# Performance work log

Measured on AMD Instinct MI355X. Metric: run time of the kernel, lower is better.

Reference implementation:

```python
import jax, jax.numpy as jnp
import numpy as np

NX, NQ, NU, NY = 256, 64, 8, 4
N = 65536
EPS = 0.01
STD = 0.5


def setup_inputs() -> dict:
    key = jax.random.key(0)
    ks = jax.random.split(key, 8)
    return {
        "x": jax.random.normal(ks[0], (N, NX), jnp.float32),
        "u": jax.random.normal(ks[1], (N, NU), jnp.float32),
        "X": jax.random.normal(ks[2], (NX + NQ, NX + NQ), jnp.float32) * STD,
        "U": jax.random.normal(ks[3], (NX, NQ), jnp.float32) * STD,
        "Y1": jax.random.normal(ks[4], (NX, NX), jnp.float32) * STD,
        "XP": jax.random.normal(ks[5], (NX, NX), jnp.float32) * STD,
        "B2": jax.random.normal(ks[6], (NX, NU), jnp.float32) * STD,
        "D12": jax.random.normal(ks[7], (NQ, NU), jnp.float32) * STD,
        "bv": jnp.zeros((NQ,), jnp.float32),
        "t": 0,
    }


def _constrained(X, U, Y1, XP):
    # updateParameters(): build A, B1, C1, D11 from unconstrained params.
    P = XP @ XP.T + EPS * jnp.eye(NX, dtype=XP.dtype)
    H = X @ X.T + EPS * jnp.eye(NX + NQ, dtype=X.dtype)
    H11, H12, H22 = H[:NX, :NX], H[:NX, NX:], H[NX:, NX:]
    Y = -0.5 * (H11 + Y1 - Y1.T)
    Pinv = jnp.linalg.inv(P)
    A = Pinv @ Y                                   # [nx, nx]
    lam = 0.5 * jnp.diagonal(H22)                  # Lambda diagonal
    D11 = -jnp.tril(H22, -1) / lam[:, None]        # strictly lower triangular [nq, nq]
    C1 = U.T / lam[:, None]                        # [nq, nx]
    B1 = Pinv @ (-H12 - U)                         # [nx, nq]
    return A, B1, C1, D11


def _calc_w(base, D11):
    # Forward substitution: w_i = relu(base_i + sum_{j<i} D11[i,j] * w_j).
    # D11 is strictly lower triangular and unfilled w columns are zero, so a
    # full matvec against the carry is exact.
    nq = base.shape[1]

    def step(w, inp):
        i, row, b_col = inp                        # row: [nq], b_col: [Nbatch]
        wi = jax.nn.relu(b_col + w @ row)
        return w.at[:, i].set(wi), None

    w0 = jnp.zeros_like(base)
    w, _ = jax.lax.scan(step, w0, (jnp.arange(nq), D11, base.T))
    return w


def reference(x, u, X, U, Y1, XP, B2, D12, bv, t):
    A, B1, C1, D11 = _constrained(X, U, Y1, XP)
    base = x @ C1.T + u @ D12.T + bv               # [N, nq]
    w = _calc_w(base, D11)
    x_dot = x @ A.T + w @ B1.T + u @ B2.T          # [N, nx]
    return x_dot
```

## Files before the change

### kernel.cpp

```cpp
#include <hip/hip_runtime.h>

#define EPS_C 0.01f

typedef __attribute__((ext_vector_type(8))) short short8;
typedef __attribute__((ext_vector_type(4))) float f32x4;
typedef __attribute__((ext_vector_type(4))) unsigned short u16x4;
typedef __attribute__((ext_vector_type(8))) unsigned short u16x8;

#define WS_H    0
#define WS_C    102400
#define WS_C2   167936
#define WS_Y    233472
#define WS_RHS  299008
#define WS_D11  331776
#define WS_WFH  419840
#define WS_WFM  464896
#define WS_WFL  509952
#define WS_BBH  555008
#define WS_BBM  564224
#define WS_BBL  573440
#define WS_WG   582656
#define WS_E    4776960

__device__ __forceinline__ unsigned short f2bf(float f) {
    unsigned int u = __float_as_uint(f);
    unsigned int r = (u + 0x7fffu + ((u >> 16) & 1u)) >> 16;
    return (unsigned short)r;
}
__device__ __forceinline__ float bf2f(unsigned short h) {
    return __uint_as_float(((unsigned int)h) << 16);
}
__device__ __forceinline__ void split1(float f, unsigned short& h, unsigned short& m, unsigned short& l) {
    h = f2bf(f);
    float r1 = f - bf2f(h);
    m = f2bf(r1);
    l = f2bf(r1 - bf2f(m));
}
__device__ __forceinline__ void split8(const float* v, short8& h8, short8& m8, short8& l8) {
#pragma unroll
    for (int j = 0; j < 8; ++j) {
        unsigned short h, m, l;
        split1(v[j], h, m, l);
        h8[j] = (short)h; m8[j] = (short)m; l8[j] = (short)l;
    }
}

__global__ void k_build(const float* __restrict__ Xm, const float* __restrict__ XPm,
                        float* __restrict__ H, float* __restrict__ P) {
    int idx = blockIdx.x * 256 + threadIdx.x;
    if (idx < 102400) {
        int i = idx / 320, j = idx - i * 320;
        const float4* a = (const float4*)(Xm + i * 320);
        const float4* b = (const float4*)(Xm + j * 320);
        float s = 0.f;
        for (int k = 0; k < 80; ++k) {
            float4 va = a[k], vb = b[k];
            s += va.x * vb.x + va.y * vb.y + va.z * vb.z + va.w * vb.w;
        }
        H[idx] = (i == j) ? s + EPS_C : s;
    } else {
        idx -= 102400;
        if (idx < 65536) {
            int i = idx >> 8, j = idx & 255;
            const float4* a = (const float4*)(XPm + i * 256);
            const float4* b = (const float4*)(XPm + j * 256);
            float s = 0.f;
            for (int k = 0; k < 64; ++k) {
                float4 va = a[k], vb = b[k];
                s += va.x * vb.x + va.y * vb.y + va.z * vb.z + va.w * vb.w;
            }
            P[idx] = (i == j) ? s + EPS_C : s;
        }
    }
}

__global__ void k_derived(const float* __restrict__ H, const float* __restrict__ Um,
                          const float* __restrict__ Y1, const float* __restrict__ B2,
                          const float* __restrict__ D12,
                          float* __restrict__ Y, float* __restrict__ RHS,
                          float* __restrict__ D11g,
                          unsigned short* __restrict__ Bh, unsigned short* __restrict__ Bm,
                          unsigned short* __restrict__ Bl,
                          unsigned short* __restrict__ Bbh, unsigned short* __restrict__ Bbm,
                          unsigned short* __restrict__ Bbl) {
    int idx = blockIdx.x * 256 + threadIdx.x;
    if (idx < 65536) {
        int i = idx >> 8, j = idx & 255;
        Y[idx] = -0.5f * (H[i * 320 + j] + Y1[i * 256 + j] - Y1[j * 256 + i]);
        return;
    }
    idx -= 65536;
    if (idx < 16384) {
        RHS[idx] = -H[(idx >> 6) * 320 + 256 + (idx & 63)] - Um[idx];
        return;
    }
    idx -= 16384;
    if (idx < 4096) {
        int q = idx >> 6, j = idx & 63;
        float lam = 0.5f * H[(256 + q) * 320 + 256 + q];
        D11g[idx] = (j < q) ? -H[(256 + q) * 320 + 256 + j] / lam : 0.f;
        return;
    }
    idx -= 4096;
    if (idx < 8192) {
        int o = idx >> 5, cc = idx & 31;
        float f = (cc < 8) ? B2[o * 8 + cc] : 0.f;
        unsigned short h, m, l;
        split1(f, h, m, l);
        size_t off = (size_t)o * 352 + 256 + cc;
        Bh[off] = h; Bm[off] = m; Bl[off] = l;
        return;
    }
    idx -= 8192;
    if (idx < 18432) {
        int q = idx / 288, k = idx - q * 288;
        float f;
        if (k < 256) {
            float lam = 0.5f * H[(256 + q) * 320 + 256 + q];
            f = Um[(size_t)k * 64 + q] / lam;
        } else if (k < 264) f = D12[(size_t)q * 8 + (k - 256)];
        else f = 0.f;
        unsigned short h, m, l;
        split1(f, h, m, l);
        Bbh[idx] = h; Bbm[idx] = m; Bbl[idx] = l;
    }
}

__global__ void __launch_bounds__(256) k_inv8(const float* __restrict__ Cold, float* __restrict__ E, int b) {
    __shared__ __align__(16) float M[64 * 68];
    __shared__ __align__(16) float Rs[8 * 68];
    __shared__ __align__(16) float Ts[64 * 8];
    __shared__ float E8s[8 * 9];
    const int tid = threadIdx.x;
    const int ti = tid & 15, tj = tid >> 4;
#pragma unroll
    for (int t = 0; t < 4; ++t) {
        int e = tid + t * 256;
        int r = e >> 4, c4 = e & 15;
        float4 v = *(const float4*)&Cold[(size_t)(b * 64 + r) * 256 + b * 64 + c4 * 4];
        *(float4*)&M[r * 68 + c4 * 4] = v;
    }
    __syncthreads();
    for (int s = 0; s < 8; ++s) {
        if (tid < 64) {
            const int lane = tid;
            float e8[8];
#pragma unroll
            for (int j = 0; j < 8; ++j) e8[j] = 0.f;
            if (lane < 8) {
#pragma unroll
                for (int j = 0; j < 8; ++j) e8[j] = M[(s * 8 + lane) * 68 + s * 8 + j];
            }
#pragma unroll
            for (int k = 0; k < 8; ++k) {
                const float p = __shfl(e8[k], k);
                const float rinv = 1.0f / p;
                const float f = -e8[k] * rinv;
                const bool isk = (lane == k);
#pragma unroll
                for (int j = 0; j < 8; ++j) {
                    const float prj = __shfl(e8[j], k);
                    if (j == k) e8[j] = isk ? rinv : f;
                    else        e8[j] = isk ? prj * rinv : fmaf(f, prj, e8[j]);
                }
            }
            if (lane < 8) {
#pragma unroll
                for (int j = 0; j < 8; ++j) E8s[lane * 9 + j] = e8[j];
            }
        }
        __syncthreads();
#pragma unroll
        for (int t = 0; t < 2; ++t) {
            int e = tid + t * 256;
            int r = e >> 6, c = e & 63;
            Rs[r * 68 + c] = M[(s * 8 + r) * 68 + c];
        }
#pragma unroll
        for (int t = 0; t < 2; ++t) {
            int e = tid + t * 256;
            int i = e >> 3, c = e & 7;
            float acc = 0.f;
#pragma unroll
            for (int j = 0; j < 8; ++j) acc = fmaf(M[i * 68 + s * 8 + j], E8s[j * 9 + c], acc);
            Ts[i * 8 + c] = acc;
        }
        __syncthreads();
        {
            const bool rowIn = ((ti >> 1) == s);
            const bool colIn = ((tj >> 1) == s);
            const int i0 = ti * 4, j0 = tj * 4;
            float nv[4][4];
            if (rowIn && colIn) {
#pragma unroll
                for (int r = 0; r < 4; ++r)
#pragma unroll
                    for (int d = 0; d < 4; ++d)
                        nv[r][d] = E8s[(i0 - s * 8 + r) * 9 + (j0 - s * 8 + d)];
            } else if (rowIn) {
#pragma unroll
                for (int r = 0; r < 4; ++r)
#pragma unroll
                    for (int d = 0; d < 4; ++d) {
                        float acc = 0.f;
#pragma unroll
                        for (int c = 0; c < 8; ++c)
                            acc = fmaf(E8s[(i0 - s * 8 + r) * 9 + c], Rs[c * 68 + j0 + d], acc);
                        nv[r][d] = acc;
                    }
            } else if (colIn) {
#pragma unroll
                for (int r = 0; r < 4; ++r)
#pragma unroll
                    for (int d = 0; d < 4; ++d)
                        nv[r][d] = -Ts[(i0 + r) * 8 + (j0 - s * 8 + d)];
            } else {
#pragma unroll
                for (int r = 0; r < 4; ++r)
#pragma unroll
                    for (int d = 0; d < 4; ++d) {
                        float acc = M[(i0 + r) * 68 + j0 + d];
#pragma unroll
                        for (int c = 0; c < 8; ++c)
                            acc = fmaf(-Ts[(i0 + r) * 8 + c], Rs[c * 68 + j0 + d], acc);
                        nv[r][d] = acc;
                    }
            }
#pragma unroll
            for (int r = 0; r < 4; ++r)
#pragma unroll
                for (int d = 0; d < 4; ++d) M[(i0 + r) * 68 + j0 + d] = nv[r][d];
        }
        __syncthreads();
    }
#pragma unroll
    for (int t = 0; t < 4; ++t) {
        int e = tid + t * 256;
        int r = e >> 4, c4 = e & 15;
        float4 v = *(const float4*)&M[r * 68 + c4 * 4];
        *(float4*)&E[(size_t)r * 64 + c4 * 4] = v;
    }
}

__global__ void __launch_bounds__(256) k_gjS(const float* __restrict__ Cold, float* __restrict__ Cnew,
                                             float* __restrict__ E, int b, int nb) {
    const int I = blockIdx.x >> 2, J = blockIdx.x & 3;
    const int tid = threadIdx.x;
    const int ti = tid & 15, tj = tid >> 4;
    if (I == b && J == b) {
        const int r = tid >> 2, seg = tid & 3;
#pragma unroll
        for (int t = 0; t < 4; ++t) {
            float4 v = *(const float4*)&E[(size_t)r * 64 + seg * 16 + t * 4];
            *(float4*)&Cnew[(size_t)(b * 64 + r) * 256 + b * 64 + seg * 16 + t * 4] = v;
        }
        return;
    }
    __shared__ __align__(16) float Es[64 * 68];
    __shared__ __align__(16) float S1[64 * 68];
    __shared__ __align__(16) float S2[64 * 68];
    for (int e = tid; e < 1024; e += 256) {
        int r = e >> 4, c4 = e & 15;
        float4 v = *(const float4*)&E[(size_t)r * 64 + c4 * 4];
        *(float4*)&Es[r * 68 + c4 * 4] = v;
    }
    if (I == b) {
        for (int e = tid; e < 1024; e += 256) {
            int r = e >> 4, c4 = e & 15;
            float4 v = *(const float4*)&Cold[(size_t)(b * 64 + r) * 256 + J * 64 + c4 * 4];
            *(float4*)&S1[r * 68 + c4 * 4] = v;
        }
        __syncthreads();
        float acc[4][4];
#pragma unroll
        for (int r = 0; r < 4; ++r)
#pragma unroll
            for (int d = 0; d < 4; ++d) acc[r][d] = 0.f;
        for (int mm = 0; mm < 64; ++mm) {
            float a4[4], b4[4];
#pragma unroll
            for (int d = 0; d < 4; ++d) { a4[d] = Es[(ti * 4 + d) * 68 + mm]; b4[d] = S1[mm * 68 + tj * 4 + d]; }
#pragma unroll
            for (int r = 0; r < 4; ++r)
#pragma unroll
                for (int d = 0; d < 4; ++d) acc[r][d] = fmaf(a4[r], b4[d], acc[r][d]);
        }
#pragma unroll
        for (int r = 0; r < 4; ++r) {
            float4 v = {acc[r][0], acc[r][1], acc[r][2], acc[r][3]};
            *(float4*)&Cnew[(size_t)(b * 64 + ti * 4 + r) * 256 + J * 64 + tj * 4] = v;
        }
        return;
    }
    if (J == b) {
        for (int e = tid; e < 1024; e += 256) {
            int r = e >> 4, c4 = e & 15;
            float4 v = *(const float4*)&Cold[(size_t)(I * 64 + r) * 256 + b * 64 + c4 * 4];
            *(float4*)&S1[r * 68 + c4 * 4] = v;
        }
        __syncthreads();
        float acc[4][4];
#pragma unroll
        for (int r = 0; r < 4; ++r)
#pragma unroll
            for (int d = 0; d < 4; ++d) acc[r][d] = 0.f;
        for (int kk = 0; kk < 64; ++kk) {
            float a4[4], b4[4];
#pragma unroll
            for (int d = 0; d < 4; ++d) { a4[d] = S1[(ti * 4 + d) * 68 + kk]; b4[d] = Es[kk * 68 + tj * 4 + d]; }
#pragma unroll
            for (int r = 0; r < 4; ++r)
#pragma unroll
                for (int d = 0; d < 4; ++d) acc[r][d] = fmaf(a4[r], b4[d], acc[r][d]);
        }
#pragma unroll
        for (int r = 0; r < 4; ++r) {
            float4 v = {-acc[r][0], -acc[r][1], -acc[r][2], -acc[r][3]};
            *(float4*)&Cnew[(size_t)(I * 64 + ti * 4 + r) * 256 + b * 64 + tj * 4] = v;
        }
        return;
    }
    for (int e = tid; e < 1024; e += 256) {
        int r = e >> 4, c4 = e & 15;
        float4 v = *(const float4*)&Cold[(size_t)(I * 64 + r) * 256 + b * 64 + c4 * 4];
        *(float4*)&S1[r * 68 + c4 * 4] = v;
        float4 w = *(const float4*)&Cold[(size_t)(b * 64 + r) * 256 + J * 64 + c4 * 4];
        *(float4*)&S2[r * 68 + c4 * 4] = w;
    }
    __syncthreads();
    float t4[4][4];
#pragma unroll
    for (int r = 0; r < 4; ++r)
#pragma unroll
        for (int d = 0; d < 4; ++d) t4[r][d] = 0.f;
    for (int kk = 0; kk < 64; ++kk) {
        float a4[4], b4[4];
#pragma unroll
        for (int d = 0; d < 4; ++d) { a4[d] = S1[(ti * 4 + d) * 68 + kk]; b4[d] = Es[kk * 68 + tj * 4 + d]; }
#pragma unroll
        for (int r = 0; r < 4; ++r)
#pragma unroll
            for (int d = 0; d < 4; ++d) t4[r][d] = fmaf(a4[r], b4[d], t4[r][d]);
    }
    __syncthreads();
#pragma unroll
    for (int r = 0; r < 4; ++r)
#pragma unroll
        for (int d = 0; d < 4; ++d) S1[(ti * 4 + r) * 68 + tj * 4 + d] = t4[r][d];
    __syncthreads();
    float acc[4][4];
#pragma unroll
    for (int r = 0; r < 4; ++r) {
        float4 cv = *(const float4*)&Cold[(size_t)(I * 64 + ti * 4 + r) * 256 + J * 64 + tj * 4];
        acc[r][0] = cv.x; acc[r][1] = cv.y; acc[r][2] = cv.z; acc[r][3] = cv.w;
    }
    for (int kk = 0; kk < 64; ++kk) {
        float a4[4], b4[4];
#pragma unroll
        for (int d = 0; d < 4; ++d) { a4[d] = S1[(ti * 4 + d) * 68 + kk]; b4[d] = S2[kk * 68 + tj * 4 + d]; }
#pragma unroll
        for (int r = 0; r < 4; ++r)
#pragma unroll
            for (int d = 0; d < 4; ++d) acc[r][d] = fmaf(-a4[r], b4[d], acc[r][d]);
    }
#pragma unroll
    for (int r = 0; r < 4; ++r) {
        float4 v = {acc[r][0], acc[r][1], acc[r][2], acc[r][3]};
        *(float4*)&Cnew[(size_t)(I * 64 + ti * 4 + r) * 256 + J * 64 + tj * 4] = v;
    }
    if (I == nb && J == nb) {
        float* M   = Es;
        float* Rs2 = S2;
        float* Ts2 = S2 + 1024;
        float* E8s = S2 + 1664;
        __syncthreads();
#pragma unroll
        for (int r = 0; r < 4; ++r)
#pragma unroll
            for (int d = 0; d < 4; ++d)
                M[(ti * 4 + r) * 68 + tj * 4 + d] = acc[r][d];
        __syncthreads();
        for (int s = 0; s < 8; ++s) {
            if (tid < 64) {
                const int lane = tid;
                float e8[8];
#pragma unroll
                for (int j = 0; j < 8; ++j) e8[j] = 0.f;
                if (lane < 8) {
#pragma unroll
                    for (int j = 0; j < 8; ++j) e8[j] = M[(s * 8 + lane) * 68 + s * 8 + j];
                }
#pragma unroll
                for (int k = 0; k < 8; ++k) {
                    const float p = __shfl(e8[k], k);
                    const float rinv = 1.0f / p;
                    const float f = -e8[k] * rinv;
                    const bool isk = (lane == k);
#pragma unroll
                    for (int j = 0; j < 8; ++j) {
                        const float prj = __shfl(e8[j], k);
                        if (j == k) e8[j] = isk ? rinv : f;
                        else        e8[j] = isk ? prj * rinv : fmaf(f, prj, e8[j]);
                    }
                }
                if (lane < 8) {
#pragma unroll
                    for (int j = 0; j < 8; ++j) E8s[lane * 9 + j] = e8[j];
                }
            }
            __syncthreads();
#pragma unroll
            for (int t = 0; t < 2; ++t) {
                int e = tid + t * 256;
                int r = e >> 6, c = e & 63;
                Rs2[r * 68 + c] = M[(s * 8 + r) * 68 + c];
            }
#pragma unroll
            for (int t = 0; t < 2; ++t) {
                int e = tid + t * 256;
                int i = e >> 3, c = e & 7;
                float a2 = 0.f;
#pragma unroll
                for (int j = 0; j < 8; ++j) a2 = fmaf(M[i * 68 + s * 8 + j], E8s[j * 9 + c], a2);
                Ts2[i * 8 + c] = a2;
            }
            __syncthreads();
            {
                const bool rowIn = ((ti >> 1) == s);
                const bool colIn = ((tj >> 1) == s);
                const int i0 = ti * 4, j0 = tj * 4;
                float nv[4][4];
                if (rowIn && colIn) {
#pragma unroll
                    for (int r = 0; r < 4; ++r)
#pragma unroll
                        for (int d = 0; d < 4; ++d)
                            nv[r][d] = E8s[(i0 - s * 8 + r) * 9 + (j0 - s * 8 + d)];
                } else if (rowIn) {
#pragma unroll
                    for (int r = 0; r < 4; ++r)
#pragma unroll
                        for (int d = 0; d < 4; ++d) {
                            float a2 = 0.f;
#pragma unroll
                            for (int c = 0; c < 8; ++c)
                                a2 = fmaf(E8s[(i0 - s * 8 + r) * 9 + c], Rs2[c * 68 + j0 + d], a2);
                            nv[r][d] = a2;
                        }
                } else if (colIn) {
#pragma unroll
                    for (int r = 0; r < 4; ++r)
#pragma unroll
                        for (int d = 0; d < 4; ++d)
                            nv[r][d] = -Ts2[(i0 + r) * 8 + (j0 - s * 8 + d)];
                } else {
#pragma unroll
                    for (int r = 0; r < 4; ++r)
#pragma unroll
                        for (int d = 0; d < 4; ++d) {
                            float a2 = M[(i0 + r) * 68 + j0 + d];
#pragma unroll
                            for (int c = 0; c < 8; ++c)
                                a2 = fmaf(-Ts2[(i0 + r) * 8 + c], Rs2[c * 68 + j0 + d], a2);
                            nv[r][d] = a2;
                        }
                }
#pragma unroll
                for (int r = 0; r < 4; ++r)
#pragma unroll
                    for (int d = 0; d < 4; ++d) M[(i0 + r) * 68 + j0 + d] = nv[r][d];
            }
            __syncthreads();
        }
#pragma unroll
        for (int t = 0; t < 4; ++t) {
            int e = tid + t * 256;
            int r = e >> 4, c4 = e & 15;
            float4 v = *(const float4*)&M[r * 68 + c4 * 4];
            *(float4*)&E[(size_t)r * 64 + c4 * 4] = v;
        }
    }
}

__global__ void __launch_bounds__(256) k_apply2(const float* __restrict__ PI, const float* __restrict__ Y,
                                                const float* __restrict__ RHS,
                                                unsigned short* __restrict__ Bh, unsigned short* __restrict__ Bm,
                                                unsigned short* __restrict__ Bl) {
    const int i0 = ((int)blockIdx.x / 5) * 64;
    const int c0 = ((int)blockIdx.x % 5) * 64;
    __shared__ __align__(16) float S1[64 * 68], S2[64 * 68];
    const int tid = threadIdx.x;
    const int ti = tid & 15, tj = tid >> 4;
    float acc[4][4];
#pragma unroll
    for (int r = 0; r < 4; ++r)
#pragma unroll
        for (int d = 0; d < 4; ++d) acc[r][d] = 0.f;
    for (int kc = 0; kc < 4; ++kc) {
        __syncthreads();
        for (int e = tid; e < 1024; e += 256) {
            int i = e >> 4, k4 = e & 15;
            float4 v = *(const float4*)&PI[(size_t)(i0 + i) * 256 + kc * 64 + k4 * 4];
            S1[(k4 * 4 + 0) * 68 + i] = v.x;
            S1[(k4 * 4 + 1) * 68 + i] = v.y;
            S1[(k4 * 4 + 2) * 68 + i] = v.z;
            S1[(k4 * 4 + 3) * 68 + i] = v.w;
            float4 w;
            if (c0 < 256) w = *(const float4*)&Y[(size_t)(kc * 64 + i) * 256 + c0 + k4 * 4];
            else          w = *(const float4*)&RHS[(size_t)(kc * 64 + i) * 64 + k4 * 4];
            *(float4*)&S2[i * 68 + k4 * 4] = w;
        }
        __syncthreads();
        for (int kk = 0; kk < 64; ++kk) {
            float4 pv = *(const float4*)&S1[kk * 68 + ti * 4];
            float4 gv = *(const float4*)&S2[kk * 68 + tj * 4];
            float p4[4] = {pv.x, pv.y, pv.z, pv.w};
            float g4[4] = {gv.x, gv.y, gv.z, gv.w};
#pragma unroll
            for (int r = 0; r < 4; ++r)
#pragma unroll
                for (int d = 0; d < 4; ++d) acc[r][d] = fmaf(p4[r], g4[d], acc[r][d]);
        }
    }
    const int pc0 = (c0 < 256) ? c0 : 288;
#pragma unroll
    for (int r = 0; r < 4; ++r)
#pragma unroll
        for (int d = 0; d < 4; ++d) {
            unsigned short h, m, l;
            split1(acc[r][d], h, m, l);
            size_t off = (size_t)(i0 + ti * 4 + r) * 352 + pc0 + tj * 4 + d;
            Bh[off] = h; Bm[off] = m; Bl[off] = l;
        }
}

#define XSTR 264
__global__ void __launch_bounds__(256, 3) k_base(const float* __restrict__ x, const float* __restrict__ u,
                                                 const unsigned short* __restrict__ Bbh,
                                                 const unsigned short* __restrict__ Bbm,
                                                 const unsigned short* __restrict__ Bbl,
                                                 const float* __restrict__ bv,
                                                 float* __restrict__ wg) {
    __shared__ __align__(16) unsigned short Ah[32 * XSTR];
    __shared__ __align__(16) unsigned short Am[32 * XSTR];
    __shared__ __align__(16) unsigned short Al[32 * XSTR];
    const int tid = threadIdx.x;
    const int r0 = blockIdx.x * 32;
    {
        const float4* xg4 = (const float4*)(x + (size_t)r0 * 256);
#pragma unroll
        for (int i = 0; i < 8; ++i) {
            int e = tid + i * 256, r = e >> 6, c4 = e & 63;
            float4 v = xg4[e];
            float vv[4] = {v.x, v.y, v.z, v.w};
            u16x4 hv, mv, lv;
#pragma unroll
            for (int j = 0; j < 4; ++j) {
                unsigned short h, m, l;
                split1(vv[j], h, m, l);
                hv[j] = h; mv[j] = m; lv[j] = l;
            }
            *(u16x4*)&Ah[r * XSTR + c4 * 4] = hv;
            *(u16x4*)&Am[r * XSTR + c4 * 4] = mv;
            *(u16x4*)&Al[r * XSTR + c4 * 4] = lv;
        }
    }
    __syncthreads();
    const int lane = tid & 63, wid = tid >> 6;
    const int n0 = wid * 16;
    const int lr = lane & 15, lg = lane >> 4;
    const int lk = lg * 8;
    const int noff = (n0 + lr) * 288;
    f32x4 acc[2];
    acc[0] = (f32x4){0.f, 0.f, 0.f, 0.f};
    acc[1] = (f32x4){0.f, 0.f, 0.f, 0.f};
    short8 cb_h, nb_h, b_m, b_l;
    cb_h = *(const short8*)&Bbh[noff + lk];
#pragma unroll
    for (int kt = 0; kt < 9; ++kt) {
        const int ka = kt * 32 + lk;
        b_m = *(const short8*)&Bbm[noff + ka];
        b_l = *(const short8*)&Bbl[noff + ka];
        if (kt < 8) nb_h = *(const short8*)&Bbh[noff + ka + 32];
        short8 a_h[2], a_m[2], a_l[2];
        if (kt < 8) {
            a_h[0] = *(const short8*)&Ah[lr * XSTR + ka];
            a_h[1] = *(const short8*)&Ah[(16 + lr) * XSTR + ka];
            a_m[0] = *(const short8*)&Am[lr * XSTR + ka];
            a_m[1] = *(const short8*)&Am[(16 + lr) * XSTR + ka];
            a_l[0] = *(const short8*)&Al[lr * XSTR + ka];
            a_l[1] = *(const short8*)&Al[(16 + lr) * XSTR + ka];
        } else {
            if (lg == 0) {
                float vv[8];
                const float4* up = (const float4*)&u[(size_t)(r0 + lr) * 8];
                float4 v0 = up[0], v1 = up[1];
                vv[0] = v0.x; vv[1] = v0.y; vv[2] = v0.z; vv[3] = v0.w;
                vv[4] = v1.x; vv[5] = v1.y; vv[6] = v1.z; vv[7] = v1.w;
                split8(vv, a_h[0], a_m[0], a_l[0]);
                const float4* up2 = (const float4*)&u[(size_t)(r0 + 16 + lr) * 8];
                float4 w0 = up2[0], w1 = up2[1];
                vv[0] = w0.x; vv[1] = w0.y; vv[2] = w0.z; vv[3] = w0.w;
                vv[4] = w1.x; vv[5] = w1.y; vv[6] = w1.z; vv[7] = w1.w;
                split8(vv, a_h[1], a_m[1], a_l[1]);
            } else {
                short8 z = {0, 0, 0, 0, 0, 0, 0, 0};
                a_h[0] = z; a_h[1] = z; a_m[0] = z; a_m[1] = z; a_l[0] = z; a_l[1] = z;
            }
        }
#pragma unroll
        for (int m = 0; m < 2; ++m) {
            acc[m] = __builtin_amdgcn_mfma_f32_16x16x32_bf16(a_h[m], cb_h, acc[m], 0, 0, 0);
            acc[m] = __builtin_amdgcn_mfma_f32_16x16x32_bf16(a_m[m], cb_h, acc[m], 0, 0, 0);
            acc[m] = __builtin_amdgcn_mfma_f32_16x16x32_bf16(a_l[m], cb_h, acc[m], 0, 0, 0);
        }
#pragma unroll
        for (int m = 0; m < 2; ++m) {
            acc[m] = __builtin_amdgcn_mfma_f32_16x16x32_bf16(a_h[m], b_m, acc[m], 0, 0, 0);
            acc[m] = __builtin_amdgcn_mfma_f32_16x16x32_bf16(a_m[m], b_m, acc[m], 0, 0, 0);
        }
#pragma unroll
        for (int m = 0; m < 2; ++m)
            acc[m] = __builtin_amdgcn_mfma_f32_16x16x32_bf16(a_h[m], b_l, acc[m], 0, 0, 0);
        if (kt < 8) cb_h = nb_h;
    }
    const float bvv = bv[n0 + lr];
#pragma unroll
    for (int m = 0; m < 2; ++m)
#pragma unroll
        for (int j = 0; j < 4; ++j)
            wg[(size_t)(r0 + m * 16 + lg * 4 + j) * 64 + n0 + lr] = acc[m][j] + bvv;
}

__global__ void __launch_bounds__(256) k_rec(float* __restrict__ wg, const float* __restrict__ D11g) {
    __shared__ float D[64 * 64];
    const int tid = threadIdx.x;
#pragma unroll
    for (int t = 0; t < 16; ++t) D[tid + t * 256] = D11g[tid + t * 256];
    __syncthreads();
    const size_t r = (size_t)blockIdx.x * 256 + tid;
    float w[64];
    float* wr = wg + r * 64;
#pragma unroll
    for (int c = 0; c < 16; ++c) {
        float4 v = *(const float4*)&wr[c * 4];
        w[4 * c] = v.x; w[4 * c + 1] = v.y; w[4 * c + 2] = v.z; w[4 * c + 3] = v.w;
    }
    w[0] = fmaxf(w[0], 0.f);
#pragma unroll
    for (int i = 1; i < 64; ++i) {
        float s0 = w[i], s1 = 0.f, s2 = 0.f, s3 = 0.f;
#pragma unroll
        for (int j = 0; j + 3 < i; j += 4) {
            s0 = fmaf(w[j + 0], D[i * 64 + j + 0], s0);
            s1 = fmaf(w[j + 1], D[i * 64 + j + 1], s1);
            s2 = fmaf(w[j + 2], D[i * 64 + j + 2], s2);
            s3 = fmaf(w[j + 3], D[i * 64 + j + 3], s3);
        }
#pragma unroll
        for (int j = i & ~3; j < i; ++j) s0 = fmaf(w[j], D[i * 64 + j], s0);
        w[i] = fmaxf((s0 + s1) + (s2 + s3), 0.f);
    }
#pragma unroll
    for (int c = 0; c < 16; ++c) {
        float4 v = {w[4 * c], w[4 * c + 1], w[4 * c + 2], w[4 * c + 3]};
        *(float4*)&wr[c * 4] = v;
    }
}

__global__ void __launch_bounds__(256, 3) k_m2(const float* __restrict__ x, const float* __restrict__ wg,
                                               const float* __restrict__ u,
                                               const unsigned short* __restrict__ Bh,
                                               const unsigned short* __restrict__ Bm,
                                               const unsigned short* __restrict__ Bl,
                                               float* __restrict__ out) {
    __shared__ __align__(16) unsigned short Ah[32 * XSTR];
    __shared__ __align__(16) unsigned short Am[32 * XSTR];
    __shared__ __align__(16) unsigned short Al[32 * XSTR];
    const int tid = threadIdx.x;
    const int r0 = blockIdx.x * 32;
    {
        const float4* xg4 = (const float4*)(x + (size_t)r0 * 256);
#pragma unroll
        for (int i = 0; i < 8; ++i) {
            int e = tid + i * 256, r = e >> 6, c4 = e & 63;
            float4 v = xg4[e];
            float vv[4] = {v.x, v.y, v.z, v.w};
            u16x4 hv, mv, lv;
#pragma unroll
            for (int j = 0; j < 4; ++j) {
                unsigned short h, m, l;
                split1(vv[j], h, m, l);
                hv[j] = h; mv[j] = m; lv[j] = l;
            }
            *(u16x4*)&Ah[r * XSTR + c4 * 4] = hv;
            *(u16x4*)&Am[r * XSTR + c4 * 4] = mv;
            *(u16x4*)&Al[r * XSTR + c4 * 4] = lv;
        }
    }
    __syncthreads();
    const int lane = tid & 63, wid = tid >> 6;
    const int n0 = wid * 64;
    const int lr = lane & 15, lg = lane >> 4;
    const int lk = lg * 8;
    int noff[4];
#pragma unroll
    for (int nf = 0; nf < 4; ++nf) noff[nf] = (n0 + nf * 16 + lr) * 352;
    f32x4 acc[2][4];
#pragma unroll
    for (int m = 0; m < 2; ++m)
#pragma unroll
        for (int nf = 0; nf < 4; ++nf) acc[m][nf] = (f32x4){0.f, 0.f, 0.f, 0.f};
    short8 cb_h[4], nb_h[4], b_m[4], b_l[4];
#pragma unroll
    for (int nf = 0; nf < 4; ++nf) cb_h[nf] = *(const short8*)&Bh[noff[nf] + lk];
#pragma unroll
    for (int kt = 0; kt < 11; ++kt) {
        const int ka = kt * 32 + lk;
#pragma unroll
        for (int nf = 0; nf < 4; ++nf) b_m[nf] = *(const short8*)&Bm[noff[nf] + ka];
#pragma unroll
        for (int nf = 0; nf < 4; ++nf) b_l[nf] = *(const short8*)&Bl[noff[nf] + ka];
        if (kt < 10) {
#pragma unroll
            for (int nf = 0; nf < 4; ++nf) nb_h[nf] = *(const short8*)&Bh[noff[nf] + ka + 32];
        }
        short8 a_h[2], a_m[2], a_l[2];
        if (kt < 8) {
            a_h[0] = *(const short8*)&Ah[lr * XSTR + ka];
            a_h[1] = *(const short8*)&Ah[(16 + lr) * XSTR + ka];
            a_m[0] = *(const short8*)&Am[lr * XSTR + ka];
            a_m[1] = *(const short8*)&Am[(16 + lr) * XSTR + ka];
            a_l[0] = *(const short8*)&Al[lr * XSTR + ka];
            a_l[1] = *(const short8*)&Al[(16 + lr) * XSTR + ka];
        } else if (kt == 8) {
            if (lg == 0) {
                float vv[8];
                const float4* up = (const float4*)&u[(size_t)(r0 + lr) * 8];
                float4 v0 = up[0], v1 = up[1];
                vv[0] = v0.x; vv[1] = v0.y; vv[2] = v0.z; vv[3] = v0.w;
                vv[4] = v1.x; vv[5] = v1.y; vv[6] = v1.z; vv[7] = v1.w;
                split8(vv, a_h[0], a_m[0], a_l[0]);
                const float4* up2 = (const float4*)&u[(size_t)(r0 + 16 + lr) * 8];
                float4 w0 = up2[0], w1 = up2[1];
                vv[0] = w0.x; vv[1] = w0.y; vv[2] = w0.z; vv[3] = w0.w;
                vv[4] = w1.x; vv[5] = w1.y; vv[6] = w1.z; vv[7] = w1.w;
                split8(vv, a_h[1], a_m[1], a_l[1]);
            } else {
                short8 z = {0, 0, 0, 0, 0, 0, 0, 0};
                a_h[0] = z; a_h[1] = z; a_m[0] = z; a_m[1] = z; a_l[0] = z; a_l[1] = z;
            }
        } else {
            const int wc = (kt - 9) * 32 + lk;
            float vv[8];
            const float4* wp = (const float4*)&wg[(size_t)(r0 + lr) * 64 + wc];
            float4 v0 = wp[0], v1 = wp[1];
            vv[0] = v0.x; vv[1] = v0.y; vv[2] = v0.z; vv[3] = v0.w;
            vv[4] = v1.x; vv[5] = v1.y; vv[6] = v1.z; vv[7] = v1.w;
            split8(vv, a_h[0], a_m[0], a_l[0]);
            const float4* wp2 = (const float4*)&wg[(size_t)(r0 + 16 + lr) * 64 + wc];
            float4 w0 = wp2[0], w1 = wp2[1];
            vv[0] = w0.x; vv[1] = w0.y; vv[2] = w0.z; vv[3] = w0.w;
            vv[4] = w1.x; vv[5] = w1.y; vv[6] = w1.z; vv[7] = w1.w;
            split8(vv, a_h[1], a_m[1], a_l[1]);
        }
#pragma unroll
        for (int nf = 0; nf < 4; ++nf)
#pragma unroll
            for (int m = 0; m < 2; ++m) {
                acc[m][nf] = __builtin_amdgcn_mfma_f32_16x16x32_bf16(a_h[m], cb_h[nf], acc[m][nf], 0, 0, 0);
                acc[m][nf] = __builtin_amdgcn_mfma_f32_16x16x32_bf16(a_m[m], cb_h[nf], acc[m][nf], 0, 0, 0);
                acc[m][nf] = __builtin_amdgcn_mfma_f32_16x16x32_bf16(a_l[m], cb_h[nf], acc[m][nf], 0, 0, 0);
            }
#pragma unroll
        for (int nf = 0; nf < 4; ++nf)
#pragma unroll
            for (int m = 0; m < 2; ++m) {
                acc[m][nf] = __builtin_amdgcn_mfma_f32_16x16x32_bf16(a_h[m], b_m[nf], acc[m][nf], 0, 0, 0);
                acc[m][nf] = __builtin_amdgcn_mfma_f32_16x16x32_bf16(a_m[m], b_m[nf], acc[m][nf], 0, 0, 0);
                if (kt >= 9)
                    acc[m][nf] = __builtin_amdgcn_mfma_f32_16x16x32_bf16(a_l[m], b_m[nf], acc[m][nf], 0, 0, 0);
            }
#pragma unroll
        for (int nf = 0; nf < 4; ++nf)
#pragma unroll
            for (int m = 0; m < 2; ++m) {
                acc[m][nf] = __builtin_amdgcn_mfma_f32_16x16x32_bf16(a_h[m], b_l[nf], acc[m][nf], 0, 0, 0);
                if (kt >= 9)
                    acc[m][nf] = __builtin_amdgcn_mfma_f32_16x16x32_bf16(a_m[m], b_l[nf], acc[m][nf], 0, 0, 0);
            }
        if (kt < 10) {
#pragma unroll
            for (int nf = 0; nf < 4; ++nf) cb_h[nf] = nb_h[nf];
        }
    }
#pragma unroll
    for (int m = 0; m < 2; ++m)
#pragma unroll
        for (int nf = 0; nf < 4; ++nf)
#pragma unroll
            for (int j = 0; j < 4; ++j)
                out[(size_t)(r0 + m * 16 + lg * 4 + j) * 256 + n0 + nf * 16 + lr] = acc[m][nf][j];
}

extern "C" void kernel_launch(void* const* d_in, const int* in_sizes, int n_in,
                              void* d_out, int out_size, void* d_ws, size_t ws_size,
                              hipStream_t stream) {
    const float* x   = (const float*)d_in[0];
    const float* u   = (const float*)d_in[1];
    const float* Xm  = (const float*)d_in[2];
    const float* Um  = (const float*)d_in[3];
    const float* Y1  = (const float*)d_in[4];
    const float* XPm = (const float*)d_in[5];
    const float* B2  = (const float*)d_in[6];
    const float* D12 = (const float*)d_in[7];
    const float* bv  = (const float*)d_in[8];
    float* out = (float*)d_out;
    float* ws  = (float*)d_ws;

    float* H    = ws + WS_H;
    float* C0   = ws + WS_C;
    float* C1   = ws + WS_C2;
    float* Y    = ws + WS_Y;
    float* RHS  = ws + WS_RHS;
    float* D11g = ws + WS_D11;
    float* E    = ws + WS_E;
    unsigned short* Bh  = (unsigned short*)(ws + WS_WFH);
    unsigned short* Bm  = (unsigned short*)(ws + WS_WFM);
    unsigned short* Bl  = (unsigned short*)(ws + WS_WFL);
    unsigned short* Bbh = (unsigned short*)(ws + WS_BBH);
    unsigned short* Bbm = (unsigned short*)(ws + WS_BBM);
    unsigned short* Bbl = (unsigned short*)(ws + WS_BBL);
    float* wg = ws + WS_WG;

    k_build<<<656, 256, 0, stream>>>(Xm, XPm, H, C0);
    k_derived<<<441, 256, 0, stream>>>(H, Um, Y1, B2, D12, Y, RHS, D11g,
                                       Bh, Bm, Bl, Bbh, Bbm, Bbl);
    k_base<<<2048, 256, 0, stream>>>(x, u, Bbh, Bbm, Bbl, bv, wg);
    k_rec<<<256, 256, 0, stream>>>(wg, D11g);
    k_inv8<<<1, 256, 0, stream>>>(C0, E, 0);
    k_gjS<<<16, 256, 0, stream>>>(C0, C1, E, 0, 1);
    k_gjS<<<16, 256, 0, stream>>>(C1, C0, E, 1, 2);
    k_gjS<<<16, 256, 0, stream>>>(C0, C1, E, 2, 3);
    k_gjS<<<16, 256, 0, stream>>>(C1, C0, E, 3, -1);
    k_apply2<<<20, 256, 0, stream>>>(C0, Y, RHS, Bh, Bm, Bl);
    k_m2<<<2048, 256, 0, stream>>>(x, wg, u, Bh, Bm, Bl, out);
}
```

Before: 373.6 us.

## Pre-swizzle split-bf16 weight fragments into MFMA order and double-buffer GJ pivot block

Weight split arrays (Bh/Bm/Bl and Bbh/Bbm/Bbl) are now stored in a fragment-tiled layout matching the 16x16x32 MFMA operand order, so each lane's 8-element load is contiguous and coalesced instead of striding across 352/288-element rows. The k_m2 and k_base loops drop the manual prefetch of the next high part and load all three parts per k-tile. The MFMA term order is regrouped, and the last two k-tiles of k_m2 now include the a_m·b_l and a_l·b_m terms. The Gauss-Jordan pivot inverse E is ping-ponged between two buffers to avoid a read/write hazard across blocks. Dropping the software prefetch may expose global load latency.

After: 340.7 us. -8.8%, faster.

```diff
diff --git a/kernel.cpp b/kernel.cpp
--- a/kernel.cpp
+++ b/kernel.cpp
@@ -20,7 +20,15 @@
 #define WS_BBM  564224
 #define WS_BBL  573440
 #define WS_WG   582656
-#define WS_E    4776960
+#define WS_E0   4776960
+#define WS_E1   4781056
+
+__device__ __forceinline__ int wfoff(int n, int k) {
+    return (((n >> 4) * 44 + (k >> 5) * 4 + ((k >> 3) & 3)) << 7) + ((n & 15) << 3) + (k & 7);
+}
+__device__ __forceinline__ int bboff(int n, int k) {
+    return (((n >> 4) * 36 + (k >> 5) * 4 + ((k >> 3) & 3)) << 7) + ((n & 15) << 3) + (k & 7);
+}
 
 __device__ __forceinline__ unsigned short f2bf(float f) {
     unsigned int u = __float_as_uint(f);
@@ -107,7 +115,7 @@
         float f = (cc < 8) ? B2[o * 8 + cc] : 0.f;
         unsigned short h, m, l;
         split1(f, h, m, l);
-        size_t off = (size_t)o * 352 + 256 + cc;
+        int off = wfoff(o, 256 + cc);
         Bh[off] = h; Bm[off] = m; Bl[off] = l;
         return;
     }
@@ -122,7 +130,8 @@
         else f = 0.f;
         unsigned short h, m, l;
         split1(f, h, m, l);
-        Bbh[idx] = h; Bbm[idx] = m; Bbl[idx] = l;
+        int off = bboff(q, k);
+        Bbh[off] = h; Bbm[off] = m; Bbl[off] = l;
     }
 }
 
@@ -243,7 +252,8 @@
 }
 
 __global__ void __launch_bounds__(256) k_gjS(const float* __restrict__ Cold, float* __restrict__ Cnew,
-                                             float* __restrict__ E, int b, int nb) {
+                                             const float* __restrict__ E, float* __restrict__ Eout,
+                                             int b, int nb) {
     const int I = blockIdx.x >> 2, J = blockIdx.x & 3;
     const int tid = threadIdx.x;
     const int ti = tid & 15, tj = tid >> 4;
@@ -477,7 +487,7 @@
             int e = tid + t * 256;
             int r = e >> 4, c4 = e & 15;
             float4 v = *(const float4*)&M[r * 68 + c4 * 4];
-            *(float4*)&E[(size_t)r * 64 + c4 * 4] = v;
+            *(float4*)&Eout[(size_t)r * 64 + c4 * 4] = v;
         }
     }
 }
@@ -529,7 +539,7 @@
         for (int d = 0; d < 4; ++d) {
             unsigned short h, m, l;
             split1(acc[r][d], h, m, l);
-            size_t off = (size_t)(i0 + ti * 4 + r) * 352 + pc0 + tj * 4 + d;
+            int off = wfoff(i0 + ti * 4 + r, pc0 + tj * 4 + d);
             Bh[off] = h; Bm[off] = m; Bl[off] = l;
         }
 }
@@ -570,18 +580,12 @@
     const int n0 = wid * 16;
     const int lr = lane & 15, lg = lane >> 4;
     const int lk = lg * 8;
-    const int noff = (n0 + lr) * 288;
+    const int fb = wid * 4608 + lg * 128 + lr * 8;
     f32x4 acc[2];
     acc[0] = (f32x4){0.f, 0.f, 0.f, 0.f};
     acc[1] = (f32x4){0.f, 0.f, 0.f, 0.f};
-    short8 cb_h, nb_h, b_m, b_l;
-    cb_h = *(const short8*)&Bbh[noff + lk];
-#pragma unroll
     for (int kt = 0; kt < 9; ++kt) {
         const int ka = kt * 32 + lk;
-        b_m = *(const short8*)&Bbm[noff + ka];
-        b_l = *(const short8*)&Bbl[noff + ka];
-        if (kt < 8) nb_h = *(const short8*)&Bbh[noff + ka + 32];
         short8 a_h[2], a_m[2], a_l[2];
         if (kt < 8) {
             a_h[0] = *(const short8*)&Ah[lr * XSTR + ka];
@@ -608,21 +612,19 @@
                 a_h[0] = z; a_h[1] = z; a_m[0] = z; a_m[1] = z; a_l[0] = z; a_l[1] = z;
             }
         }
+        const int off = fb + kt * 512;
+        short8 b_h = *(const short8*)&Bbh[off];
+        short8 b_m = *(const short8*)&Bbm[off];
+        short8 b_l = *(const short8*)&Bbl[off];
 #pragma unroll
         for (int m = 0; m < 2; ++m) {
-            acc[m] = __builtin_amdgcn_mfma_f32_16x16x32_bf16(a_h[m], cb_h, acc[m], 0, 0, 0);
-            acc[m] = __builtin_amdgcn_mfma_f32_16x16x32_bf16(a_m[m], cb_h, acc[m], 0, 0, 0);
-            acc[m] = __builtin_amdgcn_mfma_f32_16x16x32_bf16(a_l[m], cb_h, acc[m], 0, 0, 0);
-        }
-#pragma unroll
-        for (int m = 0; m < 2; ++m) {
+            acc[m] = __builtin_amdgcn_mfma_f32_16x16x32_bf16(a_h[m], b_h, acc[m], 0, 0, 0);
+            acc[m] = __builtin_amdgcn_mfma_f32_16x16x32_bf16(a_m[m], b_h, acc[m], 0, 0, 0);
             acc[m] = __builtin_amdgcn_mfma_f32_16x16x32_bf16(a_h[m], b_m, acc[m], 0, 0, 0);
+            acc[m] = __builtin_amdgcn_mfma_f32_16x16x32_bf16(a_l[m], b_h, acc[m], 0, 0, 0);
             acc[m] = __builtin_amdgcn_mfma_f32_16x16x32_bf16(a_m[m], b_m, acc[m], 0, 0, 0);
-        }
-#pragma unroll
-        for (int m = 0; m < 2; ++m)
             acc[m] = __builtin_amdgcn_mfma_f32_16x16x32_bf16(a_h[m], b_l, acc[m], 0, 0, 0);
-        if (kt < 8) cb_h = nb_h;
+        }
     }
     const float bvv = bv[n0 + lr];
 #pragma unroll
@@ -703,55 +705,81 @@
     const int n0 = wid * 64;
     const int lr = lane & 15, lg = lane >> 4;
     const int lk = lg * 8;
-    int noff[4];
-#pragma unroll
-    for (int nf = 0; nf < 4; ++nf) noff[nf] = (n0 + nf * 16 + lr) * 352;
+    const int lgoff = lg * 128 + lr * 8;
+    int fb[4];
+#pragma unroll
+    for (int nf = 0; nf < 4; ++nf) fb[nf] = (wid * 4 + nf) * 5632 + lgoff;
     f32x4 acc[2][4];
 #pragma unroll
     for (int m = 0; m < 2; ++m)
 #pragma unroll
         for (int nf = 0; nf < 4; ++nf) acc[m][nf] = (f32x4){0.f, 0.f, 0.f, 0.f};
-    short8 cb_h[4], nb_h[4], b_m[4], b_l[4];
-#pragma unroll
-    for (int nf = 0; nf < 4; ++nf) cb_h[nf] = *(const short8*)&Bh[noff[nf] + lk];
-#pragma unroll
-    for (int kt = 0; kt < 11; ++kt) {
+
+#define M2_MFMA6()                                                                               \
+    for (int nf = 0; nf < 4; ++nf) {                                                             \
+        for (int m = 0; m < 2; ++m) {                                                            \
+            acc[m][nf] = __builtin_amdgcn_mfma_f32_16x16x32_bf16(a_h[m], b_h[nf], acc[m][nf], 0, 0, 0); \
+            acc[m][nf] = __builtin_amdgcn_mfma_f32_16x16x32_bf16(a_m[m], b_h[nf], acc[m][nf], 0, 0, 0); \
+            acc[m][nf] = __builtin_amdgcn_mfma_f32_16x16x32_bf16(a_h[m], b_m[nf], acc[m][nf], 0, 0, 0); \
+            acc[m][nf] = __builtin_amdgcn_mfma_f32_16x16x32_bf16(a_l[m], b_h[nf], acc[m][nf], 0, 0, 0); \
+            acc[m][nf] = __builtin_amdgcn_mfma_f32_16x16x32_bf16(a_m[m], b_m[nf], acc[m][nf], 0, 0, 0); \
+            acc[m][nf] = __builtin_amdgcn_mfma_f32_16x16x32_bf16(a_h[m], b_l[nf], acc[m][nf], 0, 0, 0); \
+        }                                                                                        \
+    }
+
+    for (int kt = 0; kt < 8; ++kt) {
         const int ka = kt * 32 + lk;
-#pragma unroll
-        for (int nf = 0; nf < 4; ++nf) b_m[nf] = *(const short8*)&Bm[noff[nf] + ka];
-#pragma unroll
-        for (int nf = 0; nf < 4; ++nf) b_l[nf] = *(const short8*)&Bl[noff[nf] + ka];
-        if (kt < 10) {
-#pragma unroll
-            for (int nf = 0; nf < 4; ++nf) nb_h[nf] = *(const short8*)&Bh[noff[nf] + ka + 32];
-        }
         short8 a_h[2], a_m[2], a_l[2];
-        if (kt < 8) {
-            a_h[0] = *(const short8*)&Ah[lr * XSTR + ka];
-            a_h[1] = *(const short8*)&Ah[(16 + lr) * XSTR + ka];
-            a_m[0] = *(const short8*)&Am[lr * XSTR + ka];
-            a_m[1] = *(const short8*)&Am[(16 + lr) * XSTR + ka];
-            a_l[0] = *(const short8*)&Al[lr * XSTR + ka];
-            a_l[1] = *(const short8*)&Al[(16 + lr) * XSTR + ka];
-        } else if (kt == 8) {
-            if (lg == 0) {
-                float vv[8];
-                const float4* up = (const float4*)&u[(size_t)(r0 + lr) * 8];
-                float4 v0 = up[0], v1 = up[1];
-                vv[0] = v0.x; vv[1] = v0.y; vv[2] = v0.z; vv[3] = v0.w;
-                vv[4] = v1.x; vv[5] = v1.y; vv[6] = v1.z; vv[7] = v1.w;
-                split8(vv, a_h[0], a_m[0], a_l[0]);
-                const float4* up2 = (const float4*)&u[(size_t)(r0 + 16 + lr) * 8];
-                float4 w0 = up2[0], w1 = up2[1];
-                vv[0] = w0.x; vv[1] = w0.y; vv[2] = w0.z; vv[3] = w0.w;
-                vv[4] = w1.x; vv[5] = w1.y; vv[6] = w1.z; vv[7] = w1.w;
-                split8(vv, a_h[1], a_m[1], a_l[1]);
-            } else {
-                short8 z = {0, 0, 0, 0, 0, 0, 0, 0};
-                a_h[0] = z; a_h[1] = z; a_m[0] = z; a_m[1] = z; a_l[0] = z; a_l[1] = z;
-            }
+        a_h[0] = *(const short8*)&Ah[lr * XSTR + ka];
+        a_h[1] = *(const short8*)&Ah[(16 + lr) * XSTR + ka];
+        a_m[0] = *(const short8*)&Am[lr * XSTR + ka];
+        a_m[1] = *(const short8*)&Am[(16 + lr) * XSTR + ka];
+        a_l[0] = *(const short8*)&Al[lr * XSTR + ka];
+        a_l[1] = *(const short8*)&Al[(16 + lr) * XSTR + ka];
+        short8 b_h[4], b_m[4], b_l[4];
+#pragma unroll
+        for (int nf = 0; nf < 4; ++nf) {
+            const int off = fb[nf] + kt * 512;
+            b_h[nf] = *(const short8*)&Bh[off];
+            b_m[nf] = *(const short8*)&Bm[off];
+            b_l[nf] = *(const short8*)&Bl[off];
+        }
+#pragma unroll
+        M2_MFMA6()
+    }
+    {
+        short8 a_h[2], a_m[2], a_l[2];
+        if (lg == 0) {
+            float vv[8];
+            const float4* up = (const float4*)&u[(size_t)(r0 + lr) * 8];
+            float4 v0 = up[0], v1 = up[1];
+            vv[0] = v0.x; vv[1] = v0.y; vv[2] = v0.z; vv[3] = v0.w;
+            vv[4] = v1.x; vv[5] = v1.y; vv[6] = v1.z; vv[7] = v1.w;
+            split8(vv, a_h[0], a_m[0], a_l[0]);
+            const float4* up2 = (const float4*)&u[(size_t)(r0 + 16 + lr) * 8];
+            float4 w0 = up2[0], w1 = up2[1];
+            vv[0] = w0.x; vv[1] = w0.y; vv[2] = w0.z; vv[3] = w0.w;
+            vv[4] = w1.x; vv[5] = w1.y; vv[6] = w1.z; vv[7] = w1.w;
+            split8(vv, a_h[1], a_m[1], a_l[1]);
         } else {
-            const int wc = (kt - 9) * 32 + lk;
+            short8 z = {0, 0, 0, 0, 0, 0, 0, 0};
+            a_h[0] = z; a_h[1] = z; a_m[0] = z; a_m[1] = z; a_l[0] = z; a_l[1] = z;
+        }
+        short8 b_h[4], b_m[4], b_l[4];
+#pragma unroll
+        for (int nf = 0; nf < 4; ++nf) {
+            const int off = fb[nf] + 8 * 512;
+            b_h[nf] = *(const short8*)&Bh[off];
+            b_m[nf] = *(const short8*)&Bm[off];
+            b_l[nf] = *(const short8*)&Bl[off];
+        }
+#pragma unroll
+        M2_MFMA6()
+    }
+    for (int kt = 9; kt < 11; ++kt) {
+        const int wc = (kt - 9) * 32 + lk;
+        short8 a_h[2], a_m[2], a_l[2];
+        {
             float vv[8];
             const float4* wp = (const float4*)&wg[(size_t)(r0 + lr) * 64 + wc];
             float4 v0 = wp[0], v1 = wp[1];
@@ -764,34 +792,27 @@
             vv[4] = w1.x; vv[5] = w1.y; vv[6] = w1.z; vv[7] = w1.w;
             split8(vv, a_h[1], a_m[1], a_l[1]);
         }
-#pragma unroll
-        for (int nf = 0; nf < 4; ++nf)
+        short8 b_h[4], b_m[4], b_l[4];
+#pragma unroll
+        for (int nf = 0; nf < 4; ++nf) {
+            const int off = fb[nf] + kt * 512;
+            b_h[nf] = *(const short8*)&Bh[off];
+            b_m[nf] = *(const short8*)&Bm[off];
+            b_l[nf] = *(const short8*)&Bl[off];
+        }
+#pragma unroll
+        for (int nf = 0; nf < 4; ++nf) {
 #pragma unroll
             for (int m = 0; m < 2; ++m) {
-                acc[m][nf] = __builtin_amdgcn_mfma_f32_16x16x32_bf16(a_h[m], cb_h[nf], acc[m][nf], 0, 0, 0);
-                acc[m][nf] = __builtin_amdgcn_mfma_f32_16x16x32_bf16(a_m[m], cb_h[nf], acc[m][nf], 0, 0, 0);
-                acc[m][nf] = __builtin_amdgcn_mfma_f32_16x16x32_bf16(a_l[m], cb_h[nf], acc[m][nf], 0, 0, 0);
-            }
-#pragma unroll
-        for (int nf = 0; nf < 4; ++nf)
-#pragma unroll
-            for (int m = 0; m < 2; ++m) {
+                acc[m][nf] = __builtin_amdgcn_mfma_f32_16x16x32_bf16(a_h[m], b_h[nf], acc[m][nf], 0, 0, 0);
+                acc[m][nf] = __builtin_amdgcn_mfma_f32_16x16x32_bf16(a_m[m], b_h[nf], acc[m][nf], 0, 0, 0);
                 acc[m][nf] = __builtin_amdgcn_mfma_f32_16x16x32_bf16(a_h[m], b_m[nf], acc[m][nf], 0, 0, 0);
+                acc[m][nf] = __builtin_amdgcn_mfma_f32_16x16x32_bf16(a_l[m], b_h[nf], acc[m][nf], 0, 0, 0);
                 acc[m][nf] = __builtin_amdgcn_mfma_f32_16x16x32_bf16(a_m[m], b_m[nf], acc[m][nf], 0, 0, 0);
-                if (kt >= 9)
-                    acc[m][nf] = __builtin_amdgcn_mfma_f32_16x16x32_bf16(a_l[m], b_m[nf], acc[m][nf], 0, 0, 0);
-            }
-#pragma unroll
-        for (int nf = 0; nf < 4; ++nf)
-#pragma unroll
-            for (int m = 0; m < 2; ++m) {
                 acc[m][nf] = __builtin_amdgcn_mfma_f32_16x16x32_bf16(a_h[m], b_l[nf], acc[m][nf], 0, 0, 0);
-                if (kt >= 9)
-                    acc[m][nf] = __builtin_amdgcn_mfma_f32_16x16x32_bf16(a_m[m], b_l[nf], acc[m][nf], 0, 0, 0);
-            }
-        if (kt < 10) {
-#pragma unroll
-            for (int nf = 0; nf < 4; ++nf) cb_h[nf] = nb_h[nf];
+                acc[m][nf] = __builtin_amdgcn_mfma_f32_16x16x32_bf16(a_m[m], b_l[nf], acc[m][nf], 0, 0, 0);
+                acc[m][nf] = __builtin_amdgcn_mfma_f32_16x16x32_bf16(a_l[m], b_m[nf], acc[m][nf], 0, 0, 0);
+            }
         }
     }
 #pragma unroll
@@ -824,7 +845,8 @@
     float* Y    = ws + WS_Y;
     float* RHS  = ws + WS_RHS;
     float* D11g = ws + WS_D11;
-    float* E    = ws + WS_E;
+    float* E0   = ws + WS_E0;
+    float* E1   = ws + WS_E1;
     unsigned short* Bh  = (unsigned short*)(ws + WS_WFH);
     unsigned short* Bm  = (unsigned short*)(ws + WS_WFM);
     unsigned short* Bl  = (unsigned short*)(ws + WS_WFL);
@@ -838,11 +860,11 @@
                                        Bh, Bm, Bl, Bbh, Bbm, Bbl);
     k_base<<<2048, 256, 0, stream>>>(x, u, Bbh, Bbm, Bbl, bv, wg);
     k_rec<<<256, 256, 0, stream>>>(wg, D11g);
-    k_inv8<<<1, 256, 0, stream>>>(C0, E, 0);
-    k_gjS<<<16, 256, 0, stream>>>(C0, C1, E, 0, 1);
-    k_gjS<<<16, 256, 0, stream>>>(C1, C0, E, 1, 2);
-    k_gjS<<<16, 256, 0, stream>>>(C0, C1, E, 2, 3);
-    k_gjS<<<16, 256, 0, stream>>>(C1, C0, E, 3, -1);
+    k_inv8<<<1, 256, 0, stream>>>(C0, E0, 0);
+    k_gjS<<<16, 256, 0, stream>>>(C0, C1, E0, E1, 0, 1);
+    k_gjS<<<16, 256, 0, stream>>>(C1, C0, E1, E0, 1, 2);
+    k_gjS<<<16, 256, 0, stream>>>(C0, C1, E0, E1, 2, 3);
+    k_gjS<<<16, 256, 0, stream>>>(C1, C0, E1, E0, 3, -1);
     k_apply2<<<20, 256, 0, stream>>>(C0, Y, RHS, Bh, Bm, Bl);
     k_m2<<<2048, 256, 0, stream>>>(x, wg, u, Bh, Bm, Bl, out);
 }
```
